# Kernel optimization log

Hardware: AMD Instinct MI355X
Metric: run time of the kernel (lower is better)

## Reference

```python
import jax, jax.numpy as jnp
import numpy as np

KS = 3   # deform conv kernel size
PAD = 1  # deform conv padding


def conv2d(x, w, b=None, stride=1, pad=0):
    out = jax.lax.conv_general_dilated(
        x, w, (stride, stride), [(pad, pad), (pad, pad)],
        dimension_numbers=('NCHW', 'OIHW', 'NCHW'))
    if b is not None:
        out = out + b[None, :, None, None]
    return out


def batchnorm(x, g, b, eps=1e-5):
    # training-mode BN (batch statistics, biased variance) like torch default
    m = jnp.mean(x, axis=(0, 2, 3), keepdims=True)
    v = jnp.var(x, axis=(0, 2, 3), keepdims=True)
    return (x - m) * jax.lax.rsqrt(v + eps) * g[None, :, None, None] + b[None, :, None, None]


def deform_conv(x, offset, w):
    # x: (b,c,h,w); offset: (b,2N,h,w) with first N = x-offsets, last N = y-offsets
    b, c, h, wd = x.shape
    N = KS * KS
    xp = jnp.pad(x, ((0, 0), (0, 0), (PAD, PAD), (PAD, PAD)))
    Hp, Wp = h + 2 * PAD, wd + 2 * PAD
    # kernel-point offsets p_n in {-1,0,1}^2
    r = jnp.arange(-(KS - 1) // 2, (KS - 1) // 2 + 1)
    pnx, pny = jnp.meshgrid(r, r, indexing='ij')
    p_n = jnp.concatenate([pnx.reshape(-1), pny.reshape(-1)]).astype(x.dtype)  # (2N,)
    # base sampling grid p_0 (1..h, 1..w in padded coords)
    p0x, p0y = jnp.meshgrid(jnp.arange(1, h + 1), jnp.arange(1, wd + 1), indexing='ij')
    p0 = jnp.concatenate([jnp.broadcast_to(p0x[None], (N, h, wd)),
                          jnp.broadcast_to(p0y[None], (N, h, wd))], 0).astype(x.dtype)
    p = p0[None] + p_n[None, :, None, None] + offset          # (b,2N,h,w)
    p = jnp.transpose(p, (0, 2, 3, 1))                        # (b,h,w,2N)
    px, py = p[..., :N], p[..., N:]
    fx, fy = jnp.floor(px), jnp.floor(py)
    q_ltx = jnp.clip(fx, 0, Hp - 1)
    q_lty = jnp.clip(fy, 0, Wp - 1)
    q_rbx = jnp.clip(fx + 1, 0, Hp - 1)
    q_rby = jnp.clip(fy + 1, 0, Wp - 1)
    # out-of-bound positions snapped to floor, then clamped (matches torch ref)
    mx = (px < PAD) | (px > Hp - 1 - PAD)
    my = (py < PAD) | (py > Wp - 1 - PAD)
    px = jnp.clip(jnp.where(mx, fx, px), 0, Hp - 1)
    py = jnp.clip(jnp.where(my, fy, py), 0, Wp - 1)
    g_lt = (1 + (q_ltx - px)) * (1 + (q_lty - py))
    g_rb = (1 - (q_rbx - px)) * (1 - (q_rby - py))
    g_lb = (1 + (q_ltx - px)) * (1 - (q_rby - py))
    g_rt = (1 - (q_rbx - px)) * (1 + (q_lty - py))
    x_flat = xp.reshape(b, c, Hp * Wp)

    def gather(qx, qy):
        idx = (qx.astype(jnp.int32) * Wp + qy.astype(jnp.int32)).reshape(b, 1, -1)
        out = jnp.take_along_axis(x_flat, jnp.broadcast_to(idx, (b, c, idx.shape[-1])), axis=2)
        return out.reshape(b, c, h, wd, N)

    x_off = (g_lt[:, None] * gather(q_ltx, q_lty)
             + g_rb[:, None] * gather(q_rbx, q_rby)
             + g_lb[:, None] * gather(q_ltx, q_rby)
             + g_rt[:, None] * gather(q_rbx, q_lty))   # (b,c,h,w,N)
    # (b,c,h,w,ki,kj) -> (b,c,h*ks,w*ks), then conv with stride ks
    x_off = x_off.reshape(b, c, h, wd, KS, KS).transpose(0, 1, 2, 4, 3, 5).reshape(b, c, h * KS, wd * KS)
    return conv2d(x_off, w, None, stride=KS, pad=0)


def setup_inputs() -> dict:
    key = jax.random.key(0)
    ks = jax.random.split(key, 6)
    f32 = jnp.float32
    x = jax.random.normal(ks[0], (4, 3, 224, 224), f32)
    conv1_w = jax.random.normal(ks[1], (64, 3, 3, 3), f32) * (1.0 / np.sqrt(3 * 9))
    conv1_b = jnp.zeros((64,), f32)
    bn1_g = jnp.ones((64,), f32); bn1_b = jnp.zeros((64,), f32)
    conv2_w = jax.random.normal(ks[2], (128, 64, 3, 3), f32) * (1.0 / np.sqrt(64 * 9))
    conv2_b = jnp.zeros((128,), f32)
    bn2_g = jnp.ones((128,), f32); bn2_b = jnp.zeros((128,), f32)
    off_w = jax.random.normal(ks[3], (18, 128, 3, 3), f32) * 0.01
    off_b = jnp.zeros((18,), f32)
    conv4_w = jax.random.normal(ks[4], (128, 128, 3, 3), f32) * (1.0 / np.sqrt(128 * 9))
    return {'x': x, 'conv1_w': conv1_w, 'conv1_b': conv1_b, 'bn1_g': bn1_g, 'bn1_b': bn1_b,
            'conv2_w': conv2_w, 'conv2_b': conv2_b, 'bn2_g': bn2_g, 'bn2_b': bn2_b,
            'off_w': off_w, 'off_b': off_b, 'conv4_w': conv4_w}


def reference(x, conv1_w, conv1_b, bn1_g, bn1_b, conv2_w, conv2_b, bn2_g, bn2_b, off_w, off_b, conv4_w):
    h = jax.nn.relu(conv2d(x, conv1_w, conv1_b, pad=1))
    h = batchnorm(h, bn1_g, bn1_b)
    b_, c_, H, W = h.shape
    h = h.reshape(b_, c_, H // 2, 2, W // 2, 2).mean(axis=(3, 5))  # AvgPool2d(2,2)
    h = jax.nn.relu(conv2d(h, conv2_w, conv2_b, pad=1))
    h = batchnorm(h, bn2_g, bn2_b)
    offsets = conv2d(h, off_w, off_b, pad=1)
    return deform_conv(h, offsets, conv4_w)
```

## Files before the change

### kernel.cpp

```cpp
#include <hip/hip_runtime.h>

#define HW1 50176
#define HW2 12544

typedef short bf16x8 __attribute__((ext_vector_type(8)));
typedef float f32x4  __attribute__((ext_vector_type(4)));

static __device__ __forceinline__ unsigned short f2bf(float f) {
  union { float f; unsigned int u; } v; v.f = f;
  unsigned int u = v.u;
  return (unsigned short)((u + 0x7fffu + ((u >> 16) & 1u)) >> 16);
}
static __device__ __forceinline__ float bf2f(unsigned short h) {
  union { unsigned int u; float f; } v; v.u = ((unsigned int)h) << 16;
  return v.f;
}

__global__ __launch_bounds__(256) void conv1_tiled_kernel(
    const float* __restrict__ x, const float* __restrict__ w,
    const float* __restrict__ bias, float* __restrict__ out)
{
  __shared__ float in_s[3][18][18];
  int tid = threadIdx.x;
  int tx = tid & 15, ty = tid >> 4;
  int tx0 = (blockIdx.x % 14) * 16, ty0 = (blockIdx.x / 14) * 16;
  int b = blockIdx.y;

  for (int t = tid; t < 972; t += 256) {
    int c = t / 324, r2 = t % 324;
    int r = r2 / 18, col = r2 % 18;
    int yy = ty0 + r - 1, xx = tx0 + col - 1;
    float v = 0.f;
    if (yy >= 0 && yy < 224 && xx >= 0 && xx < 224)
      v = x[((size_t)(b * 3 + c) * 224 + yy) * 224 + xx];
    in_s[c][r][col] = v;
  }
  __syncthreads();

  float xv[27];
  #pragma unroll
  for (int c = 0; c < 3; ++c)
    #pragma unroll
    for (int ky = 0; ky < 3; ++ky)
      #pragma unroll
      for (int kx = 0; kx < 3; ++kx)
        xv[c * 9 + ky * 3 + kx] = in_s[c][ty + ky][tx + kx];

  int oy = ty0 + ty, ox = tx0 + tx;
  size_t obase = ((size_t)b * 64) * HW1 + (size_t)oy * 224 + ox;
  for (int o0 = 0; o0 < 64; o0 += 16) {
    float acc[16];
    #pragma unroll
    for (int oi = 0; oi < 16; ++oi) acc[oi] = bias[o0 + oi];
    #pragma unroll
    for (int oi = 0; oi < 16; ++oi) {
      const float* wp = w + (size_t)(o0 + oi) * 27;
      #pragma unroll
      for (int k = 0; k < 27; ++k)
        acc[oi] += xv[k] * wp[k];
    }
    #pragma unroll
    for (int oi = 0; oi < 16; ++oi)
      out[obase + (size_t)(o0 + oi) * HW1] = fmaxf(acc[oi], 0.f);
  }
}

__global__ __launch_bounds__(256) void bn_stats_kernel(
    const float* __restrict__ in, float* __restrict__ stats, int C, int HW)
{
  int c = blockIdx.y;
  float s = 0.f, s2 = 0.f;
  int stride = gridDim.x * 256;
  int start = blockIdx.x * 256 + threadIdx.x;
  for (int b = 0; b < 4; ++b) {
    const float* p = in + (size_t)(b * C + c) * HW;
    for (int i = start; i < HW; i += stride) {
      float v = p[i];
      s += v; s2 += v * v;
    }
  }
  #pragma unroll
  for (int off = 32; off > 0; off >>= 1) {
    s  += __shfl_down(s, off, 64);
    s2 += __shfl_down(s2, off, 64);
  }
  __shared__ float red[8];
  int wid = threadIdx.x >> 6, lane = threadIdx.x & 63;
  if (lane == 0) { red[wid * 2] = s; red[wid * 2 + 1] = s2; }
  __syncthreads();
  if (threadIdx.x == 0) {
    float ts = 0.f, ts2 = 0.f;
    for (int i = 0; i < 4; ++i) { ts += red[i * 2]; ts2 += red[i * 2 + 1]; }
    atomicAdd(&stats[2 * c], ts);
    atomicAdd(&stats[2 * c + 1], ts2);
  }
}

__global__ void bn_finalize_kernel(const float* __restrict__ stats,
                                   const float* __restrict__ g,
                                   const float* __restrict__ bb,
                                   float inv_n, float* __restrict__ ss, int C)
{
  int c = threadIdx.x;
  if (c < C) {
    float m = stats[2 * c] * inv_n;
    float v = stats[2 * c + 1] * inv_n - m * m;
    float sc = rsqrtf(v + 1e-5f) * g[c];
    ss[2 * c] = sc;
    ss[2 * c + 1] = bb[c] - m * sc;
  }
}

__global__ __launch_bounds__(256) void bn1_pool_nhwc_kernel(
    const float* __restrict__ h1, const float* __restrict__ ss,
    float* __restrict__ out)
{
  __shared__ float tile[16][65];
  int b = blockIdx.z, y = blockIdx.y, x0 = blockIdx.x * 16;
  int tid = threadIdx.x;
  int c = tid >> 2, g = tid & 3;
  const float2* r0 = (const float2*)(h1 + ((size_t)((b * 64 + c) * 224 + 2 * y)) * 224);
  const float2* r1 = r0 + 112;
  float sc = ss[2 * c], sh = ss[2 * c + 1];
  #pragma unroll
  for (int i = 0; i < 4; ++i) {
    int xl = g * 4 + i;
    float2 a = r0[x0 + xl], d = r1[x0 + xl];
    tile[xl][c] = (a.x + a.y + d.x + d.y) * 0.25f * sc + sh;
  }
  __syncthreads();
  int c2 = tid & 63, pg = tid >> 6;
  size_t obase = (size_t)b * HW2 + y * 112 + x0;
  #pragma unroll
  for (int i = 0; i < 4; ++i) {
    int xl = pg * 4 + i;
    out[(obase + xl) * 64 + c2] = tile[xl][c2];
  }
}

__global__ __launch_bounds__(256) void bn2_apply_nhwc_kernel(
    const float* __restrict__ h3, const float* __restrict__ ss,
    float* __restrict__ onhwc)
{
  __shared__ float tile[16][129];
  int b = blockIdx.z, y = blockIdx.y, x0 = blockIdx.x * 16;
  int tid = threadIdx.x;
  int xx = tid & 15, cbase = tid >> 4;
  #pragma unroll
  for (int it = 0; it < 8; ++it) {
    int c = cbase + it * 16;
    size_t gi = ((size_t)((b * 128 + c) * 112 + y)) * 112 + x0 + xx;
    float v = h3[gi];
    tile[xx][c] = v * ss[2 * c] + ss[2 * c + 1];
  }
  __syncthreads();
  int c2 = tid & 127, xb2 = tid >> 7;
  #pragma unroll
  for (int it = 0; it < 8; ++it) {
    int xx2 = xb2 + it * 2;
    onhwc[((size_t)((b * 112 + y) * 112) + x0 + xx2) * 128 + c2] = tile[xx2][c2];
  }
}

__global__ __launch_bounds__(256) void wprep_kernel(
    const float* __restrict__ w, unsigned short* __restrict__ wb)
{
  int t = blockIdx.x * 256 + threadIdx.x;
  if (t >= 128 * 1152) return;
  int o = t / 1152, r = t % 1152;
  int kk = r / 128, c = r % 128;
  wb[t] = f2bf(w[((size_t)o * 128 + c) * 9 + kk]);
}

__global__ __launch_bounds__(256) void wprep2s_kernel(
    const float* __restrict__ w, unsigned short* __restrict__ wh,
    unsigned short* __restrict__ wl)
{
  int t = blockIdx.x * 256 + threadIdx.x;
  if (t >= 128 * 576) return;
  int o = t / 576, r = t % 576;
  int kk = r / 64, c = r % 64;
  float v = w[((size_t)o * 64 + c) * 9 + kk];
  unsigned short h = f2bf(v);
  wh[t] = h;
  wl[t] = f2bf(v - bf2f(h));
}

__global__ __launch_bounds__(256) void wprep_offs_kernel(
    const float* __restrict__ w, unsigned short* __restrict__ wh,
    unsigned short* __restrict__ wl)
{
  int t = blockIdx.x * 256 + threadIdx.x;
  if (t >= 32 * 1152) return;
  int o = t / 1152, r = t % 1152;
  int kk = r / 128, c = r % 128;
  float v = (o < 18) ? w[((size_t)o * 128 + c) * 9 + kk] : 0.f;
  unsigned short h = f2bf(v);
  wh[t] = h;
  wl[t] = f2bf(v - bf2f(h));
}

__global__ __launch_bounds__(256) void conv2_mfma3_kernel(
    const float* __restrict__ xin, const unsigned short* __restrict__ wh,
    const unsigned short* __restrict__ wl, const float* __restrict__ bias,
    float* __restrict__ out)
{
  __shared__ unsigned short wh_lds[128 * 32];
  __shared__ unsigned short wl_lds[128 * 32];
  __shared__ unsigned short xh_lds[64 * 32];
  __shared__ unsigned short xl_lds[64 * 32];
  int tid = threadIdx.x;
  int p0 = blockIdx.x * 64;
  int b  = blockIdx.y;
  const float* xb = xin + (size_t)b * HW2 * 64;

  f32x4 acc[4][2];
  #pragma unroll
  for (int f = 0; f < 4; ++f)
    #pragma unroll
    for (int g = 0; g < 2; ++g)
      acc[f][g] = (f32x4){0.f, 0.f, 0.f, 0.f};

  int wid = tid >> 6, l = tid & 63;
  int wo = (wid & 1) * 64, wp = (wid >> 1) * 32;
  int kgl = l >> 4, rl = l & 15;

  int pl = tid >> 2, kg = tid & 3;
  int pix = p0 + pl;
  int pi = pix / 112, pj = pix % 112;

  for (int step = 0; step < 18; ++step) {
    int k0 = step * 32;
    int kk = k0 >> 6;
    __syncthreads();
    #pragma unroll
    for (int it = 0; it < 2; ++it) {
      int task = tid + it * 256;
      int row = task >> 2, wkg = task & 3;
      size_t goff = (size_t)row * 576 + k0 + wkg * 8;
      int loff = row * 32 + ((wkg ^ ((row >> 1) & 3)) << 3);
      *(bf16x8*)(wh_lds + loff) = *(const bf16x8*)(wh + goff);
      *(bf16x8*)(wl_lds + loff) = *(const bf16x8*)(wl + goff);
    }
    {
      int dy = kk / 3 - 1, dx = kk % 3 - 1;
      int yy = pi + dy, xx = pj + dx;
      int c = (k0 & 63) + kg * 8;
      bf16x8 xvh, xvl;
      if (yy >= 0 && yy < 112 && xx >= 0 && xx < 112) {
        const float4* tp = (const float4*)(xb + ((size_t)(yy * 112 + xx)) * 64 + c);
        float4 t0 = tp[0], t1 = tp[1];
        float v[8] = {t0.x, t0.y, t0.z, t0.w, t1.x, t1.y, t1.z, t1.w};
        #pragma unroll
        for (int t = 0; t < 8; ++t) {
          unsigned short hsh = f2bf(v[t]);
          xvh[t] = (short)hsh;
          xvl[t] = (short)f2bf(v[t] - bf2f(hsh));
        }
      } else {
        #pragma unroll
        for (int t = 0; t < 8; ++t) { xvh[t] = 0; xvl[t] = 0; }
      }
      int loff = pl * 32 + ((kg ^ ((pl >> 1) & 3)) << 3);
      *(bf16x8*)(xh_lds + loff) = xvh;
      *(bf16x8*)(xl_lds + loff) = xvl;
    }
    __syncthreads();
    bf16x8 ah[4], al[4], bh[2], bl[2];
    #pragma unroll
    for (int f = 0; f < 4; ++f) {
      int r = wo + f * 16 + rl;
      int loff = r * 32 + ((kgl ^ ((r >> 1) & 3)) << 3);
      ah[f] = *(const bf16x8*)(wh_lds + loff);
      al[f] = *(const bf16x8*)(wl_lds + loff);
    }
    #pragma unroll
    for (int g = 0; g < 2; ++g) {
      int r = wp + g * 16 + rl;
      int loff = r * 32 + ((kgl ^ ((r >> 1) & 3)) << 3);
      bh[g] = *(const bf16x8*)(xh_lds + loff);
      bl[g] = *(const bf16x8*)(xl_lds + loff);
    }
    #pragma unroll
    for (int f = 0; f < 4; ++f)
      #pragma unroll
      for (int g = 0; g < 2; ++g) {
        acc[f][g] = __builtin_amdgcn_mfma_f32_16x16x32_bf16(ah[f], bh[g], acc[f][g], 0, 0, 0);
        acc[f][g] = __builtin_amdgcn_mfma_f32_16x16x32_bf16(ah[f], bl[g], acc[f][g], 0, 0, 0);
        acc[f][g] = __builtin_amdgcn_mfma_f32_16x16x32_bf16(al[f], bh[g], acc[f][g], 0, 0, 0);
      }
  }

  int jrow = (l >> 4) * 4, col = l & 15;
  #pragma unroll
  for (int f = 0; f < 4; ++f) {
    #pragma unroll
    for (int g = 0; g < 2; ++g) {
      int p = p0 + wp + g * 16 + col;
      #pragma unroll
      for (int j = 0; j < 4; ++j) {
        int o = wo + f * 16 + jrow + j;
        out[((size_t)(b * 128 + o)) * HW2 + p] = fmaxf(acc[f][g][j] + bias[o], 0.f);
      }
    }
  }
}

__global__ __launch_bounds__(256) void off_mfma3_kernel(
    const float* __restrict__ xin, const unsigned short* __restrict__ wh,
    const unsigned short* __restrict__ wl, const float* __restrict__ bias,
    float* __restrict__ out)
{
  __shared__ unsigned short wh_lds[32 * 32];
  __shared__ unsigned short wl_lds[32 * 32];
  __shared__ unsigned short xh_lds[128 * 32];
  __shared__ unsigned short xl_lds[128 * 32];
  int tid = threadIdx.x;
  int p0 = blockIdx.x * 128;
  int b  = blockIdx.y;
  const float* xb = xin + (size_t)b * HW2 * 128;

  f32x4 acc[2][2];
  #pragma unroll
  for (int f = 0; f < 2; ++f)
    #pragma unroll
    for (int g = 0; g < 2; ++g)
      acc[f][g] = (f32x4){0.f, 0.f, 0.f, 0.f};

  int wid = tid >> 6, l = tid & 63;
  int wp = wid * 32;
  int kgl = l >> 4, rl = l & 15;

  for (int step = 0; step < 36; ++step) {
    int k0 = step * 32;
    int kk = k0 >> 7;
    int dy = kk / 3 - 1, dx = kk % 3 - 1;
    __syncthreads();
    if (tid < 128) {
      int row = tid >> 2, wkg = tid & 3;
      size_t goff = (size_t)row * 1152 + k0 + wkg * 8;
      int loff = row * 32 + ((wkg ^ ((row >> 1) & 3)) << 3);
      *(bf16x8*)(wh_lds + loff) = *(const bf16x8*)(wh + goff);
      *(bf16x8*)(wl_lds + loff) = *(const bf16x8*)(wl + goff);
    }
    #pragma unroll
    for (int it = 0; it < 2; ++it) {
      int task = tid + it * 256;
      int pl = task >> 2, kg = task & 3;
      int pix = p0 + pl;
      int pi = pix / 112, pj = pix % 112;
      int yy = pi + dy, xx = pj + dx;
      int c = (k0 & 127) + kg * 8;
      bf16x8 xvh, xvl;
      if (yy >= 0 && yy < 112 && xx >= 0 && xx < 112) {
        const float4* tp = (const float4*)(xb + ((size_t)(yy * 112 + xx)) * 128 + c);
        float4 t0 = tp[0], t1 = tp[1];
        float v[8] = {t0.x, t0.y, t0.z, t0.w, t1.x, t1.y, t1.z, t1.w};
        #pragma unroll
        for (int t = 0; t < 8; ++t) {
          unsigned short hsh = f2bf(v[t]);
          xvh[t] = (short)hsh;
          xvl[t] = (short)f2bf(v[t] - bf2f(hsh));
        }
      } else {
        #pragma unroll
        for (int t = 0; t < 8; ++t) { xvh[t] = 0; xvl[t] = 0; }
      }
      int loff = pl * 32 + ((kg ^ ((pl >> 1) & 3)) << 3);
      *(bf16x8*)(xh_lds + loff) = xvh;
      *(bf16x8*)(xl_lds + loff) = xvl;
    }
    __syncthreads();
    bf16x8 ah[2], al[2], bh[2], bl[2];
    #pragma unroll
    for (int f = 0; f < 2; ++f) {
      int r = f * 16 + rl;
      int loff = r * 32 + ((kgl ^ ((r >> 1) & 3)) << 3);
      ah[f] = *(const bf16x8*)(wh_lds + loff);
      al[f] = *(const bf16x8*)(wl_lds + loff);
    }
    #pragma unroll
    for (int g = 0; g < 2; ++g) {
      int r = wp + g * 16 + rl;
      int loff = r * 32 + ((kgl ^ ((r >> 1) & 3)) << 3);
      bh[g] = *(const bf16x8*)(xh_lds + loff);
      bl[g] = *(const bf16x8*)(xl_lds + loff);
    }
    #pragma unroll
    for (int f = 0; f < 2; ++f)
      #pragma unroll
      for (int g = 0; g < 2; ++g) {
        acc[f][g] = __builtin_amdgcn_mfma_f32_16x16x32_bf16(ah[f], bh[g], acc[f][g], 0, 0, 0);
        acc[f][g] = __builtin_amdgcn_mfma_f32_16x16x32_bf16(ah[f], bl[g], acc[f][g], 0, 0, 0);
        acc[f][g] = __builtin_amdgcn_mfma_f32_16x16x32_bf16(al[f], bh[g], acc[f][g], 0, 0, 0);
      }
  }

  int jrow = (l >> 4) * 4, col = l & 15;
  #pragma unroll
  for (int f = 0; f < 2; ++f) {
    #pragma unroll
    for (int g = 0; g < 2; ++g) {
      int p = p0 + wp + g * 16 + col;
      #pragma unroll
      for (int j = 0; j < 4; ++j) {
        int o = f * 16 + jrow + j;
        if (o < 18)
          out[((size_t)(b * 18 + o)) * HW2 + p] = acc[f][g][j] + bias[o];
      }
    }
  }
}

__global__ __launch_bounds__(256) void deform_mfma_kernel(
    const float* __restrict__ xin, const float* __restrict__ offs,
    const unsigned short* __restrict__ wb, float* __restrict__ out)
{
  __shared__ int            idx_s[576][4];
  __shared__ float          wt_s[576][4];
  __shared__ unsigned short w_lds[128 * 32];
  __shared__ unsigned short x_lds[64 * 32];

  int tid = threadIdx.x;
  int p0 = blockIdx.x * 64;
  int b  = blockIdx.y;
  const float* xb = xin + (size_t)b * HW2 * 128;

  for (int t = tid; t < 576; t += 256) {
    int p = t / 9, k = t % 9;
    int pix = p0 + p;
    int i = pix / 112, j = pix % 112;
    float offx = offs[((size_t)(b * 18 + k) * 112 + i) * 112 + j];
    float offy = offs[((size_t)(b * 18 + 9 + k) * 112 + i) * 112 + j];
    float px = (float)(i + k / 3) + offx;
    float py = (float)(j + k % 3) + offy;
    float fx = floorf(px), fy = floorf(py);
    float qltx = fminf(fmaxf(fx, 0.f), 113.f);
    float qlty = fminf(fmaxf(fy, 0.f), 113.f);
    float qrbx = fminf(fmaxf(fx + 1.f, 0.f), 113.f);
    float qrby = fminf(fmaxf(fy + 1.f, 0.f), 113.f);
    bool mx = (px < 1.f) || (px > 112.f);
    bool my = (py < 1.f) || (py > 112.f);
    float pxc = fminf(fmaxf(mx ? fx : px, 0.f), 113.f);
    float pyc = fminf(fmaxf(my ? fy : py, 0.f), 113.f);
    float glt = (1.f + (qltx - pxc)) * (1.f + (qlty - pyc));
    float grb = (1.f - (qrbx - pxc)) * (1.f - (qrby - pyc));
    float glb = (1.f + (qltx - pxc)) * (1.f - (qrby - pyc));
    float grt = (1.f - (qrbx - pxc)) * (1.f + (qlty - pyc));
    int ix0 = (int)qltx - 1, iy0 = (int)qlty - 1;
    int ix1 = (int)qrbx - 1, iy1 = (int)qrby - 1;
    bool vx0 = (ix0 >= 0 && ix0 < 112), vy0 = (iy0 >= 0 && iy0 < 112);
    bool vx1 = (ix1 >= 0 && ix1 < 112), vy1 = (iy1 >= 0 && iy1 < 112);
    idx_s[t][0] = (vx0 && vy0) ? ix0 * 112 + iy0 : -1;  wt_s[t][0] = glt;
    idx_s[t][1] = (vx1 && vy1) ? ix1 * 112 + iy1 : -1;  wt_s[t][1] = grb;
    idx_s[t][2] = (vx0 && vy1) ? ix0 * 112 + iy1 : -1;  wt_s[t][2] = glb;
    idx_s[t][3] = (vx1 && vy0) ? ix1 * 112 + iy0 : -1;  wt_s[t][3] = grt;
  }

  f32x4 acc[4][2];
  #pragma unroll
  for (int f = 0; f < 4; ++f)
    #pragma unroll
    for (int g = 0; g < 2; ++g)
      acc[f][g] = (f32x4){0.f, 0.f, 0.f, 0.f};

  int wid = tid >> 6;
  int l   = tid & 63;
  int wo = (wid & 1) * 64;
  int wp = (wid >> 1) * 32;
  int kgl = l >> 4;
  int rl  = l & 15;

  __syncthreads();

  for (int step = 0; step < 36; ++step) {
    int k0 = step * 32;
    int kk = k0 >> 7;
    int c0 = k0 & 127;
    __syncthreads();

    #pragma unroll
    for (int it = 0; it < 2; ++it) {
      int task = tid + it * 256;
      int row = task >> 2, kg = task & 3;
      bf16x8 wv = *(const bf16x8*)(wb + (size_t)row * 1152 + k0 + kg * 8);
      *(bf16x8*)(w_lds + row * 32 + ((kg ^ ((row >> 1) & 3)) << 3)) = wv;
    }

    {
      int pl = tid >> 2, kg = tid & 3;
      int c = c0 + kg * 8;
      int pk = pl * 9 + kk;
      float v0 = 0.f, v1 = 0.f, v2 = 0.f, v3 = 0.f;
      float v4 = 0.f, v5 = 0.f, v6 = 0.f, v7 = 0.f;
      #pragma unroll
      for (int q = 0; q < 4; ++q) {
        int s = idx_s[pk][q];
        if (s >= 0) {
          float wq = wt_s[pk][q];
          const float4* tp = (const float4*)(xb + (size_t)s * 128 + c);
          float4 t0 = tp[0], t1 = tp[1];
          v0 += wq * t0.x; v1 += wq * t0.y; v2 += wq * t0.z; v3 += wq * t0.w;
          v4 += wq * t1.x; v5 += wq * t1.y; v6 += wq * t1.z; v7 += wq * t1.w;
        }
      }
      bf16x8 xv;
      xv[0] = (short)f2bf(v0); xv[1] = (short)f2bf(v1);
      xv[2] = (short)f2bf(v2); xv[3] = (short)f2bf(v3);
      xv[4] = (short)f2bf(v4); xv[5] = (short)f2bf(v5);
      xv[6] = (short)f2bf(v6); xv[7] = (short)f2bf(v7);
      *(bf16x8*)(x_lds + pl * 32 + ((kg ^ ((pl >> 1) & 3)) << 3)) = xv;
    }
    __syncthreads();

    bf16x8 af[4], bx[2];
    #pragma unroll
    for (int f = 0; f < 4; ++f) {
      int r = wo + f * 16 + rl;
      af[f] = *(const bf16x8*)(w_lds + r * 32 + ((kgl ^ ((r >> 1) & 3)) << 3));
    }
    #pragma unroll
    for (int g = 0; g < 2; ++g) {
      int r = wp + g * 16 + rl;
      bx[g] = *(const bf16x8*)(x_lds + r * 32 + ((kgl ^ ((r >> 1) & 3)) << 3));
    }
    #pragma unroll
    for (int f = 0; f < 4; ++f)
      #pragma unroll
      for (int g = 0; g < 2; ++g)
        acc[f][g] = __builtin_amdgcn_mfma_f32_16x16x32_bf16(af[f], bx[g], acc[f][g], 0, 0, 0);
  }

  int jrow = (l >> 4) * 4;
  int col  = l & 15;
  #pragma unroll
  for (int f = 0; f < 4; ++f) {
    #pragma unroll
    for (int g = 0; g < 2; ++g) {
      #pragma unroll
      for (int j = 0; j < 4; ++j) {
        int o = wo + f * 16 + jrow + j;
        int p = p0 + wp + g * 16 + col;
        out[((size_t)(b * 128 + o)) * HW2 + p] = acc[f][g][j];
      }
    }
  }
}

extern "C" void kernel_launch(void* const* d_in, const int* in_sizes, int n_in,
                              void* d_out, int out_size, void* d_ws, size_t ws_size,
                              hipStream_t stream)
{
  const float* x       = (const float*)d_in[0];
  const float* conv1_w = (const float*)d_in[1];
  const float* conv1_b = (const float*)d_in[2];
  const float* bn1_g   = (const float*)d_in[3];
  const float* bn1_b   = (const float*)d_in[4];
  const float* conv2_w = (const float*)d_in[5];
  const float* conv2_b = (const float*)d_in[6];
  const float* bn2_g   = (const float*)d_in[7];
  const float* bn2_b   = (const float*)d_in[8];
  const float* off_w   = (const float*)d_in[9];
  const float* off_b   = (const float*)d_in[10];
  const float* conv4_w = (const float*)d_in[11];
  float* out = (float*)d_out;
  float* ws  = (float*)d_ws;

  float* bufA  = ws;
  float* bufB  = bufA + 12845056;
  float* bufC  = bufB + 3211264;
  float* offsb = bufC + 6422528;
  float* stats = offsb + 903168;
  float* ss    = stats + 384;
  unsigned short* wbf  = (unsigned short*)(ss + 384);
  unsigned short* wb2h = wbf + 147456;
  unsigned short* wb2l = wb2h + 73728;
  unsigned short* wboh = wb2l + 73728;
  unsigned short* wbol = wboh + 36864;

  float* h1  = bufA;
  float* h2t = bufB;
  float* h3  = bufA;
  float* h4t = bufC;

  hipMemsetAsync(stats, 0, 384 * sizeof(float), stream);

  wprep_kernel<<<(128 * 1152 + 255) / 256, 256, 0, stream>>>(conv4_w, wbf);
  wprep2s_kernel<<<(128 * 576 + 255) / 256, 256, 0, stream>>>(conv2_w, wb2h, wb2l);
  wprep_offs_kernel<<<(32 * 1152 + 255) / 256, 256, 0, stream>>>(off_w, wboh, wbol);

  conv1_tiled_kernel<<<dim3(196, 4), 256, 0, stream>>>(x, conv1_w, conv1_b, h1);
  bn_stats_kernel<<<dim3(32, 64), 256, 0, stream>>>(h1, stats, 64, HW1);
  bn_finalize_kernel<<<1, 128, 0, stream>>>(stats, bn1_g, bn1_b, 1.f / (4.f * HW1), ss, 64);
  bn1_pool_nhwc_kernel<<<dim3(7, 112, 4), 256, 0, stream>>>(h1, ss, h2t);

  conv2_mfma3_kernel<<<dim3(196, 4), 256, 0, stream>>>(h2t, wb2h, wb2l, conv2_b, h3);
  bn_stats_kernel<<<dim3(16, 128), 256, 0, stream>>>(h3, stats + 128, 128, HW2);
  bn_finalize_kernel<<<1, 128, 0, stream>>>(stats + 128, bn2_g, bn2_b, 1.f / (4.f * HW2), ss + 128, 128);
  bn2_apply_nhwc_kernel<<<dim3(7, 112, 4), 256, 0, stream>>>(h3, ss + 128, h4t);

  off_mfma3_kernel<<<dim3(98, 4), 256, 0, stream>>>(h4t, wboh, wbol, off_b, offsb);
  deform_mfma_kernel<<<dim3(196, 4), 256, 0, stream>>>(h4t, offsb, wbf, out);
}
```

Baseline: 371.9 us.

## Merge weight-prep kernels, drop BN atomics, swizzle block order, double deform K-step

```diff
diff --git a/kernel.cpp b/kernel.cpp
--- a/kernel.cpp
+++ b/kernel.cpp
@@ -14,6 +14,37 @@
 static __device__ __forceinline__ float bf2f(unsigned short h) {
   union { unsigned int u; float f; } v; v.u = ((unsigned int)h) << 16;
   return v.f;
+}
+
+__global__ __launch_bounds__(256) void prep_kernel(
+    const float* __restrict__ conv4_w, const float* __restrict__ conv2_w,
+    const float* __restrict__ off_w,
+    unsigned short* __restrict__ wbf, unsigned short* __restrict__ wb2h,
+    unsigned short* __restrict__ wb2l, unsigned short* __restrict__ wboh,
+    unsigned short* __restrict__ wbol)
+{
+  int t = blockIdx.x * 256 + threadIdx.x;
+  if (t < 147456) {
+    int o = t / 1152, r = t % 1152;
+    int kk = r / 128, c = r % 128;
+    wbf[t] = f2bf(conv4_w[((size_t)o * 128 + c) * 9 + kk]);
+  }
+  int t2 = t - 147456;
+  if (t2 >= 0 && t2 < 73728) {
+    int o = t2 / 576, r = t2 % 576;
+    int kk = r / 64, c = r % 64;
+    float v = conv2_w[((size_t)o * 64 + c) * 9 + kk];
+    unsigned short h = f2bf(v);
+    wb2h[t2] = h; wb2l[t2] = f2bf(v - bf2f(h));
+  }
+  int t3 = t - (147456 + 73728);
+  if (t3 >= 0 && t3 < 36864) {
+    int o = t3 / 1152, r = t3 % 1152;
+    int kk = r / 128, c = r % 128;
+    float v = (o < 18) ? off_w[((size_t)o * 128 + c) * 9 + kk] : 0.f;
+    unsigned short h = f2bf(v);
+    wboh[t3] = h; wbol[t3] = f2bf(v - bf2f(h));
+  }
 }
 
 __global__ __launch_bounds__(256) void conv1_tiled_kernel(
@@ -65,12 +96,13 @@
   }
 }
 
-__global__ __launch_bounds__(256) void bn_stats_kernel(
-    const float* __restrict__ in, float* __restrict__ stats, int C, int HW)
+__global__ __launch_bounds__(256) void bn_stats_part_kernel(
+    const float* __restrict__ in, float* __restrict__ part, int C, int HW)
 {
   int c = blockIdx.y;
+  int NB = gridDim.x;
   float s = 0.f, s2 = 0.f;
-  int stride = gridDim.x * 256;
+  int stride = NB * 256;
   int start = blockIdx.x * 256 + threadIdx.x;
   for (int b = 0; b < 4; ++b) {
     const float* p = in + (size_t)(b * C + c) * HW;
@@ -91,20 +123,25 @@
   if (threadIdx.x == 0) {
     float ts = 0.f, ts2 = 0.f;
     for (int i = 0; i < 4; ++i) { ts += red[i * 2]; ts2 += red[i * 2 + 1]; }
-    atomicAdd(&stats[2 * c], ts);
-    atomicAdd(&stats[2 * c + 1], ts2);
-  }
-}
-
-__global__ void bn_finalize_kernel(const float* __restrict__ stats,
+    part[((size_t)c * NB + blockIdx.x) * 2]     = ts;
+    part[((size_t)c * NB + blockIdx.x) * 2 + 1] = ts2;
+  }
+}
+
+__global__ void bn_finalize_kernel(const float* __restrict__ part, int NB,
                                    const float* __restrict__ g,
                                    const float* __restrict__ bb,
                                    float inv_n, float* __restrict__ ss, int C)
 {
   int c = threadIdx.x;
   if (c < C) {
-    float m = stats[2 * c] * inv_n;
-    float v = stats[2 * c + 1] * inv_n - m * m;
+    float s = 0.f, s2 = 0.f;
+    for (int i = 0; i < NB; ++i) {
+      s  += part[((size_t)c * NB + i) * 2];
+      s2 += part[((size_t)c * NB + i) * 2 + 1];
+    }
+    float m = s * inv_n;
+    float v = s2 * inv_n - m * m;
     float sc = rsqrtf(v + 1e-5f) * g[c];
     ss[2 * c] = sc;
     ss[2 * c + 1] = bb[c] - m * sc;
@@ -150,8 +187,7 @@
   for (int it = 0; it < 8; ++it) {
     int c = cbase + it * 16;
     size_t gi = ((size_t)((b * 128 + c) * 112 + y)) * 112 + x0 + xx;
-    float v = h3[gi];
-    tile[xx][c] = v * ss[2 * c] + ss[2 * c + 1];
+    tile[xx][c] = h3[gi] * ss[2 * c] + ss[2 * c + 1];
   }
   __syncthreads();
   int c2 = tid & 127, xb2 = tid >> 7;
@@ -160,44 +196,6 @@
     int xx2 = xb2 + it * 2;
     onhwc[((size_t)((b * 112 + y) * 112) + x0 + xx2) * 128 + c2] = tile[xx2][c2];
   }
-}
-
-__global__ __launch_bounds__(256) void wprep_kernel(
-    const float* __restrict__ w, unsigned short* __restrict__ wb)
-{
-  int t = blockIdx.x * 256 + threadIdx.x;
-  if (t >= 128 * 1152) return;
-  int o = t / 1152, r = t % 1152;
-  int kk = r / 128, c = r % 128;
-  wb[t] = f2bf(w[((size_t)o * 128 + c) * 9 + kk]);
-}
-
-__global__ __launch_bounds__(256) void wprep2s_kernel(
-    const float* __restrict__ w, unsigned short* __restrict__ wh,
-    unsigned short* __restrict__ wl)
-{
-  int t = blockIdx.x * 256 + threadIdx.x;
-  if (t >= 128 * 576) return;
-  int o = t / 576, r = t % 576;
-  int kk = r / 64, c = r % 64;
-  float v = w[((size_t)o * 64 + c) * 9 + kk];
-  unsigned short h = f2bf(v);
-  wh[t] = h;
-  wl[t] = f2bf(v - bf2f(h));
-}
-
-__global__ __launch_bounds__(256) void wprep_offs_kernel(
-    const float* __restrict__ w, unsigned short* __restrict__ wh,
-    unsigned short* __restrict__ wl)
-{
-  int t = blockIdx.x * 256 + threadIdx.x;
-  if (t >= 32 * 1152) return;
-  int o = t / 1152, r = t % 1152;
-  int kk = r / 128, c = r % 128;
-  float v = (o < 18) ? w[((size_t)o * 128 + c) * 9 + kk] : 0.f;
-  unsigned short h = f2bf(v);
-  wh[t] = h;
-  wl[t] = f2bf(v - bf2f(h));
 }
 
 __global__ __launch_bounds__(256) void conv2_mfma3_kernel(
@@ -210,8 +208,10 @@
   __shared__ unsigned short xh_lds[64 * 32];
   __shared__ unsigned short xl_lds[64 * 32];
   int tid = threadIdx.x;
-  int p0 = blockIdx.x * 64;
-  int b  = blockIdx.y;
+  int hw = blockIdx.y * 196 + blockIdx.x;
+  int swz = (hw & 7) * 98 + (hw >> 3);
+  int p0 = (swz % 196) * 64;
+  int b  = swz / 196;
   const float* xb = xin + (size_t)b * HW2 * 64;
 
   f32x4 acc[4][2];
@@ -316,8 +316,10 @@
   __shared__ unsigned short xh_lds[128 * 32];
   __shared__ unsigned short xl_lds[128 * 32];
   int tid = threadIdx.x;
-  int p0 = blockIdx.x * 128;
-  int b  = blockIdx.y;
+  int hw = blockIdx.y * 98 + blockIdx.x;
+  int swz = (hw & 7) * 49 + (hw >> 3);
+  int p0 = (swz % 98) * 128;
+  int b  = swz / 98;
   const float* xb = xin + (size_t)b * HW2 * 128;
 
   f32x4 acc[2][2];
@@ -418,12 +420,14 @@
 {
   __shared__ int            idx_s[576][4];
   __shared__ float          wt_s[576][4];
-  __shared__ unsigned short w_lds[128 * 32];
-  __shared__ unsigned short x_lds[64 * 32];
+  __shared__ unsigned short w_lds[128 * 64];
+  __shared__ unsigned short x_lds[64 * 64];
 
   int tid = threadIdx.x;
-  int p0 = blockIdx.x * 64;
-  int b  = blockIdx.y;
+  int hw = blockIdx.y * 196 + blockIdx.x;
+  int swz = (hw & 7) * 98 + (hw >> 3);
+  int p0 = (swz % 196) * 64;
+  int b  = swz / 196;
   const float* xb = xin + (size_t)b * HW2 * 128;
 
   for (int t = tid; t < 576; t += 256) {
@@ -471,20 +475,19 @@
   int kgl = l >> 4;
   int rl  = l & 15;
 
-  __syncthreads();
-
-  for (int step = 0; step < 36; ++step) {
-    int k0 = step * 32;
-    int kk = k0 >> 7;
-    int c0 = k0 & 127;
+  for (int step = 0; step < 18; ++step) {
+    int k0 = step * 64;
+    int kk = step >> 1;
+    int c0 = (step & 1) * 64;
     __syncthreads();
 
     #pragma unroll
-    for (int it = 0; it < 2; ++it) {
+    for (int it = 0; it < 4; ++it) {
       int task = tid + it * 256;
-      int row = task >> 2, kg = task & 3;
-      bf16x8 wv = *(const bf16x8*)(wb + (size_t)row * 1152 + k0 + kg * 8);
-      *(bf16x8*)(w_lds + row * 32 + ((kg ^ ((row >> 1) & 3)) << 3)) = wv;
+      int row = task >> 3, kg8 = task & 7;
+      int sub = kg8 >> 2, kg = kg8 & 3;
+      bf16x8 wv = *(const bf16x8*)(wb + (size_t)row * 1152 + k0 + sub * 32 + kg * 8);
+      *(bf16x8*)(w_lds + row * 64 + sub * 32 + ((kg ^ ((row >> 1) & 3)) << 3)) = wv;
     }
 
     {
@@ -493,42 +496,55 @@
       int pk = pl * 9 + kk;
       float v0 = 0.f, v1 = 0.f, v2 = 0.f, v3 = 0.f;
       float v4 = 0.f, v5 = 0.f, v6 = 0.f, v7 = 0.f;
+      float u0 = 0.f, u1 = 0.f, u2 = 0.f, u3 = 0.f;
+      float u4 = 0.f, u5 = 0.f, u6 = 0.f, u7 = 0.f;
       #pragma unroll
       for (int q = 0; q < 4; ++q) {
         int s = idx_s[pk][q];
         if (s >= 0) {
           float wq = wt_s[pk][q];
           const float4* tp = (const float4*)(xb + (size_t)s * 128 + c);
-          float4 t0 = tp[0], t1 = tp[1];
+          float4 t0 = tp[0], t1 = tp[1], t2 = tp[8], t3 = tp[9];
           v0 += wq * t0.x; v1 += wq * t0.y; v2 += wq * t0.z; v3 += wq * t0.w;
           v4 += wq * t1.x; v5 += wq * t1.y; v6 += wq * t1.z; v7 += wq * t1.w;
+          u0 += wq * t2.x; u1 += wq * t2.y; u2 += wq * t2.z; u3 += wq * t2.w;
+          u4 += wq * t3.x; u5 += wq * t3.y; u6 += wq * t3.z; u7 += wq * t3.w;
         }
       }
-      bf16x8 xv;
+      bf16x8 xv, xu;
       xv[0] = (short)f2bf(v0); xv[1] = (short)f2bf(v1);
       xv[2] = (short)f2bf(v2); xv[3] = (short)f2bf(v3);
       xv[4] = (short)f2bf(v4); xv[5] = (short)f2bf(v5);
       xv[6] = (short)f2bf(v6); xv[7] = (short)f2bf(v7);
-      *(bf16x8*)(x_lds + pl * 32 + ((kg ^ ((pl >> 1) & 3)) << 3)) = xv;
+      xu[0] = (short)f2bf(u0); xu[1] = (short)f2bf(u1);
+      xu[2] = (short)f2bf(u2); xu[3] = (short)f2bf(u3);
+      xu[4] = (short)f2bf(u4); xu[5] = (short)f2bf(u5);
+      xu[6] = (short)f2bf(u6); xu[7] = (short)f2bf(u7);
+      int sw = ((kg ^ ((pl >> 1) & 3)) << 3);
+      *(bf16x8*)(x_lds + pl * 64 + sw) = xv;
+      *(bf16x8*)(x_lds + pl * 64 + 32 + sw) = xu;
     }
     __syncthreads();
 
-    bf16x8 af[4], bx[2];
-    #pragma unroll
-    for (int f = 0; f < 4; ++f) {
-      int r = wo + f * 16 + rl;
-      af[f] = *(const bf16x8*)(w_lds + r * 32 + ((kgl ^ ((r >> 1) & 3)) << 3));
-    }
-    #pragma unroll
-    for (int g = 0; g < 2; ++g) {
-      int r = wp + g * 16 + rl;
-      bx[g] = *(const bf16x8*)(x_lds + r * 32 + ((kgl ^ ((r >> 1) & 3)) << 3));
-    }
-    #pragma unroll
-    for (int f = 0; f < 4; ++f)
-      #pragma unroll
-      for (int g = 0; g < 2; ++g)
-        acc[f][g] = __builtin_amdgcn_mfma_f32_16x16x32_bf16(af[f], bx[g], acc[f][g], 0, 0, 0);
+    #pragma unroll
+    for (int sub = 0; sub < 2; ++sub) {
+      bf16x8 af[4], bx[2];
+      #pragma unroll
+      for (int f = 0; f < 4; ++f) {
+        int r = wo + f * 16 + rl;
+        af[f] = *(const bf16x8*)(w_lds + r * 64 + sub * 32 + ((kgl ^ ((r >> 1) & 3)) << 3));
+      }
+      #pragma unroll
+      for (int g = 0; g < 2; ++g) {
+        int r = wp + g * 16 + rl;
+        bx[g] = *(const bf16x8*)(x_lds + r * 64 + sub * 32 + ((kgl ^ ((r >> 1) & 3)) << 3));
+      }
+      #pragma unroll
+      for (int f = 0; f < 4; ++f)
+        #pragma unroll
+        for (int g = 0; g < 2; ++g)
+          acc[f][g] = __builtin_amdgcn_mfma_f32_16x16x32_bf16(af[f], bx[g], acc[f][g], 0, 0, 0);
+    }
   }
 
   int jrow = (l >> 4) * 4;
@@ -570,8 +586,8 @@
   float* bufB  = bufA + 12845056;
   float* bufC  = bufB + 3211264;
   float* offsb = bufC + 6422528;
-  float* stats = offsb + 903168;
-  float* ss    = stats + 384;
+  float* part  = offsb + 903168;
+  float* ss    = part + 8192;
   unsigned short* wbf  = (unsigned short*)(ss + 384);
   unsigned short* wb2h = wbf + 147456;
   unsigned short* wb2l = wb2h + 73728;
@@ -582,21 +598,20 @@
   float* h2t = bufB;
   float* h3  = bufA;
   float* h4t = bufC;
-
-  hipMemsetAsync(stats, 0, 384 * sizeof(float), stream);
-
-  wprep_kernel<<<(128 * 1152 + 255) / 256, 256, 0, stream>>>(conv4_w, wbf);
-  wprep2s_kernel<<<(128 * 576 + 255) / 256, 256, 0, stream>>>(conv2_w, wb2h, wb2l);
-  wprep_offs_kernel<<<(32 * 1152 + 255) / 256, 256, 0, stream>>>(off_w, wboh, wbol);
+  float* part1 = part;
+  float* part2 = part + 4096;
+
+  prep_kernel<<<1008, 256, 0, stream>>>(conv4_w, conv2_w, off_w,
+                                        wbf, wb2h, wb2l, wboh, wbol);
 
   conv1_tiled_kernel<<<dim3(196, 4), 256, 0, stream>>>(x, conv1_w, conv1_b, h1);
-  bn_stats_kernel<<<dim3(32, 64), 256, 0, stream>>>(h1, stats, 64, HW1);
-  bn_finalize_kernel<<<1, 128, 0, stream>>>(stats, bn1_g, bn1_b, 1.f / (4.f * HW1), ss, 64);
+  bn_stats_part_kernel<<<dim3(32, 64), 256, 0, stream>>>(h1, part1, 64, HW1);
+  bn_finalize_kernel<<<1, 128, 0, stream>>>(part1, 32, bn1_g, bn1_b, 1.f / (4.f * HW1), ss, 64);
   bn1_pool_nhwc_kernel<<<dim3(7, 112, 4), 256, 0, stream>>>(h1, ss, h2t);
 
   conv2_mfma3_kernel<<<dim3(196, 4), 256, 0, stream>>>(h2t, wb2h, wb2l, conv2_b, h3);
-  bn_stats_kernel<<<dim3(16, 128), 256, 0, stream>>>(h3, stats + 128, 128, HW2);
-  bn_finalize_kernel<<<1, 128, 0, stream>>>(stats + 128, bn2_g, bn2_b, 1.f / (4.f * HW2), ss + 128, 128);
+  bn_stats_part_kernel<<<dim3(16, 128), 256, 0, stream>>>(h3, part2, 128, HW2);
+  bn_finalize_kernel<<<1, 128, 0, stream>>>(part2, 16, bn2_g, bn2_b, 1.f / (4.f * HW2), ss + 128, 128);
   bn2_apply_nhwc_kernel<<<dim3(7, 112, 4), 256, 0, stream>>>(h3, ss + 128, h4t);
 
   off_mfma3_kernel<<<dim3(98, 4), 256, 0, stream>>>(h4t, wboh, wbol, off_b, offsb);
```

After: 319.3 us. 14.1% less time.
